# Performance work log

Hardware: AMD Instinct MI355X
Metric: run time of the kernel (lower is better)

Reference implementation:

```python
import jax, jax.numpy as jnp
import numpy as np

B, S, HID = 16, 577, 768
H, D = 12, 64          # heads, head_dim
N_KEEP = 576           # kept channels after structured pruning


def setup_inputs() -> dict:
    key = jax.random.key(0)
    ks = jax.random.split(key, 10)
    hs = jax.random.normal(ks[0], (B, S, HID), dtype=jnp.float32)
    Wq = jax.random.normal(ks[1], (HID, N_KEEP), dtype=jnp.float32) * 0.02
    bq = jax.random.normal(ks[2], (N_KEEP,), dtype=jnp.float32) * 0.02
    Wk = jax.random.normal(ks[3], (HID, N_KEEP), dtype=jnp.float32) * 0.02
    bk = jax.random.normal(ks[4], (N_KEEP,), dtype=jnp.float32) * 0.02
    Wv = jax.random.normal(ks[5], (HID, N_KEEP), dtype=jnp.float32) * 0.02
    bv = jax.random.normal(ks[6], (N_KEEP,), dtype=jnp.float32) * 0.02
    # positions of nonzero entries of the boolean padding masks (unique, sorted)
    q_idx = jnp.sort(jax.random.permutation(ks[7], HID)[:N_KEEP]).astype(jnp.int32)
    k_idx = jnp.sort(jax.random.permutation(ks[8], HID)[:N_KEEP]).astype(jnp.int32)
    v_idx = jnp.sort(jax.random.permutation(ks[9], HID)[:N_KEEP]).astype(jnp.int32)
    return {"hidden_states": hs, "Wq": Wq, "bq": bq, "Wk": Wk, "bk": bk,
            "Wv": Wv, "bv": bv, "q_idx": q_idx, "k_idx": k_idx, "v_idx": v_idx}


def _pad_and_split_heads(x, idx):
    # scatter pruned channels [B,S,N_KEEP] back into full layout [B,S,HID],
    # then split into heads -> [B,H,S,D]
    padded = jnp.zeros((B, S, HID), dtype=x.dtype).at[:, :, idx].set(x)
    return padded.reshape(B, S, H, D).transpose(0, 2, 1, 3)


def reference(hidden_states, Wq, bq, Wk, bk, Wv, bv, q_idx, k_idx, v_idx):
    q = hidden_states @ Wq + bq            # [B,S,N_KEEP]
    k = hidden_states @ Wk + bk
    v = hidden_states @ Wv + bv
    ql = _pad_and_split_heads(q, q_idx)     # [B,H,S,D]
    kl = _pad_and_split_heads(k, k_idx)
    vl = _pad_and_split_heads(v, v_idx)
    scale = 1.0 / np.float32(np.sqrt(D))
    scores = jnp.einsum('bhqd,bhkd->bhqk', ql, kl) * scale  # [B,H,S,S]
    probs = jax.nn.softmax(scores, axis=-1)
    ctx = jnp.einsum('bhqk,bhkd->bhqd', probs, vl)          # [B,H,S,D]
    ctx = ctx.transpose(0, 2, 1, 3).reshape(B, S, HID)       # [B,S,HID]
    return ctx[:, :, v_idx]                                  # gather kept channels
```

## Files before the change

### kernel.cpp

```cpp
#include <hip/hip_runtime.h>
#include <hip/hip_bf16.h>
#include <cstdint>
#include <cstddef>

#define B_     16
#define S_     577
#define HID_   768
#define H_     12
#define D_     64
#define NKEEP_ 576
#define MROWS  (B_ * S_)
#define BHROWS (B_ * H_ * S_)

typedef __bf16 bf16;
typedef __bf16 bf16x8 __attribute__((ext_vector_type(8)));
typedef float  f32x4  __attribute__((ext_vector_type(4)));

__device__ __forceinline__ void gload16(const bf16* g, bf16* l) {
    __builtin_amdgcn_global_load_lds(
        (const __attribute__((address_space(1))) unsigned int*)g,
        (__attribute__((address_space(3))) unsigned int*)l, 16, 0, 0);
}

__global__ __launch_bounds__(256) void k_cvt(const float* __restrict__ src,
                                             bf16* __restrict__ dst, int n4) {
    int i = blockIdx.x * 256 + threadIdx.x;
    if (i >= n4) return;
    float4 v = reinterpret_cast<const float4*>(src)[i];
    union { bf16 h[4]; uint2 u; } o;
    o.h[0] = (bf16)v.x; o.h[1] = (bf16)v.y; o.h[2] = (bf16)v.z; o.h[3] = (bf16)v.w;
    reinterpret_cast<uint2*>(dst)[i] = o.u;
}

__global__ void k_inv(const int* __restrict__ qi, const int* __restrict__ ki,
                      const int* __restrict__ vi,
                      const float* __restrict__ bq, const float* __restrict__ bk,
                      const float* __restrict__ bv,
                      int* __restrict__ inv, float* __restrict__ bias_p) {
    int p = blockIdx.x, t = threadIdx.x;
    inv[p * HID_ + t] = -1;
    bias_p[p * HID_ + t] = 0.0f;
    __syncthreads();
    const int* src = (p == 0) ? qi : (p == 1) ? ki : vi;
    const float* bb = (p == 0) ? bq : (p == 1) ? bk : bv;
    if (t < NKEEP_) {
        inv[p * HID_ + src[t]] = t;
        bias_p[p * HID_ + src[t]] = bb[t];
    }
}

__global__ __launch_bounds__(256) void k_wt(const float* __restrict__ Wq,
                                            const float* __restrict__ Wk,
                                            const float* __restrict__ Wv,
                                            const int* __restrict__ qi,
                                            const int* __restrict__ ki,
                                            const int* __restrict__ vi,
                                            bf16* __restrict__ Wp_t) {
    __shared__ float tile[64][33];
    const int p = blockIdx.y;
    const int j0 = blockIdx.x * 32;
    const float* W  = (p == 0) ? Wq : (p == 1) ? Wk : Wv;
    const int* idx  = (p == 0) ? qi : (p == 1) ? ki : vi;
    bf16* dst = Wp_t + (size_t)p * HID_ * HID_;
    const int t = threadIdx.x;
    const int lj = t & 31, lk = t >> 5;
    const int sj = t >> 3, ke = (t & 7) * 8;
    const int c = idx[j0 + sj];
    for (int kt = 0; kt < HID_; kt += 64) {
        __syncthreads();
#pragma unroll
        for (int i = 0; i < 8; ++i)
            tile[lk + i * 8][lj] = W[(size_t)(kt + lk + i * 8) * NKEEP_ + j0 + lj];
        __syncthreads();
        union { bf16 h[8]; bf16x8 v; } o;
#pragma unroll
        for (int i = 0; i < 8; ++i) o.h[i] = (bf16)tile[ke + i][sj];
        *reinterpret_cast<bf16x8*>(dst + (size_t)c * HID_ + kt + ke) = o.v;
    }
}

#define BM 128
#define BN 128
#define BK 32

__global__ __launch_bounds__(256) void k_gemm(const bf16* __restrict__ X,
                                              const bf16* __restrict__ Wp_t,
                                              const float* __restrict__ bias_p,
                                              bf16* __restrict__ Qo, bf16* __restrict__ Ko,
                                              bf16* __restrict__ Vo) {
    __shared__ bf16 smem[8448];
    bf16* Asm = smem;
    bf16* Bsm = smem + 4096;

    const int L = (blockIdx.x & 7) * 180 + (blockIdx.x >> 3);
    const int m_ = L / 18, np = L % 18;
    if (m_ >= 73) return;
    const int m0 = m_ * BM;
    const int n0 = (np % 6) * BN;
    const int p  = np / 6;

    const bf16* Wbase = Wp_t + (size_t)p * HID_ * HID_;
    bf16* Obase = (p == 0) ? Qo : (p == 1) ? Ko : Vo;
    const float osc = (p == 0) ? 0.125f : 1.0f;

    const int t = threadIdx.x;
    const int wid = t >> 6, lane = t & 63;
    const int wr = wid >> 1, wc = wid & 1;
    const int lrow = lane & 15, g = lane >> 4, lk = (lane >> 4) * 8;
    const int srow = lane >> 2, scol = (lane & 3) * 8;

    f32x4 acc[4][4] = {};

    for (int kk = 0; kk < HID_; kk += BK) {
        __syncthreads();
#pragma unroll
        for (int i = 0; i < 2; ++i) {
            const int c = wid * 2 + i;
            gload16(X + (size_t)(m0 + c * 16 + srow) * HID_ + kk + scol, Asm + c * 512);
            gload16(Wbase + (size_t)(n0 + c * 16 + srow) * HID_ + kk + scol, Bsm + c * 512);
        }
        __syncthreads();

        bf16x8 af[4], bfr[4];
#pragma unroll
        for (int m = 0; m < 4; ++m)
            af[m] = *reinterpret_cast<const bf16x8*>(&Asm[(wr * 64 + m * 16 + lrow) * BK + lk]);
#pragma unroll
        for (int n = 0; n < 4; ++n)
            bfr[n] = *reinterpret_cast<const bf16x8*>(&Bsm[(wc * 64 + n * 16 + lrow) * BK + lk]);
#pragma unroll
        for (int m = 0; m < 4; ++m)
#pragma unroll
            for (int n = 0; n < 4; ++n)
                acc[m][n] = __builtin_amdgcn_mfma_f32_16x16x32_bf16(af[m], bfr[n], acc[m][n], 0, 0, 0);
    }

    float bias_n[4];
#pragma unroll
    for (int n = 0; n < 4; ++n)
        bias_n[n] = bias_p[p * HID_ + n0 + wc * 64 + n * 16 + lrow];

    const int rowl = t >> 2, cq = t & 3;
#pragma unroll
    for (int half = 0; half < 2; ++half) {
        __syncthreads();
        if (wr == half) {
#pragma unroll
            for (int n = 0; n < 4; ++n)
#pragma unroll
                for (int m = 0; m < 4; ++m)
#pragma unroll
                    for (int r = 0; r < 4; ++r)
                        smem[(m * 16 + g * 4 + r) * 132 + wc * 64 + n * 16 + lrow] =
                            (bf16)((acc[m][n][r] + bias_n[n]) * osc);
        }
        __syncthreads();
        const int grow = m0 + half * 64 + rowl;
        if (grow < MROWS) {
            const int b = grow / S_, s = grow % S_;
            const size_t rbase = ((size_t)b * H_ * S_ + s) * D_;
#pragma unroll
            for (int i = 0; i < 4; ++i) {
                const int c0 = i * 32 + cq * 8;
                bf16x8 v = *reinterpret_cast<const bf16x8*>(&smem[rowl * 132 + c0]);
                const int c = n0 + c0, h = c >> 6, d = c & 63;
                *reinterpret_cast<bf16x8*>(&Obase[rbase + (size_t)h * S_ * D_ + d]) = v;
            }
        }
    }
}

#define KB2  64
#define VLD2 72

__global__ __launch_bounds__(512, 4) void k_attn(const bf16* __restrict__ Q,
                                                 const bf16* __restrict__ K,
                                                 const bf16* __restrict__ V,
                                                 const int* __restrict__ inv,
                                                 float* __restrict__ out) {
    __shared__ bf16 Ksm[KB2 * VLD2];
    __shared__ bf16 Vsm[D_ * VLD2];

    const int bid = blockIdx.x;
    const int bh = bid % (B_ * H_);
    const int q0 = (bid / (B_ * H_)) * 128;
    const int t = threadIdx.x, wid = t >> 6, lane = t & 63;
    const int lcol = lane & 15, g = lane >> 4;

    const bf16* Qb = Q + (size_t)bh * S_ * D_;
    const bf16* Kb = K + (size_t)bh * S_ * D_;
    const bf16* Vb = V + (size_t)bh * S_ * D_;

    const int qrow = q0 + wid * 16 + lcol;
    bf16x8 qf0 = {}, qf1 = {};
    if (qrow < S_) {
        qf0 = *reinterpret_cast<const bf16x8*>(Qb + (size_t)qrow * D_ + g * 8);
        qf1 = *reinterpret_cast<const bf16x8*>(Qb + (size_t)qrow * D_ + 32 + g * 8);
    }

    const int key_t = t >> 3;
    const int a_t = t & 7;
    const int ch_t = a_t * 8;
    const int ks_s = key_t >> 4, g_s = (key_t >> 2) & 3, r_s = key_t & 3;
    const int pos = (ks_s >> 1) * 32 + g_s * 8 + (ks_s & 1) * 4 + r_s;

    float mrun = -INFINITY, lrun = 0.f;
    f32x4 oT[4] = {};
    const bf16x8 zv = {};

    bf16x8 kreg = zv, vreg = zv;
    if (key_t < S_) {
        kreg = *reinterpret_cast<const bf16x8*>(Kb + (size_t)key_t * D_ + ch_t);
        vreg = *reinterpret_cast<const bf16x8*>(Vb + (size_t)key_t * D_ + ch_t);
    }

    for (int k0 = 0; k0 < S_; k0 += KB2) {
        __syncthreads();
        *reinterpret_cast<bf16x8*>(&Ksm[key_t * VLD2 + ch_t]) = kreg;
#pragma unroll
        for (int i = 0; i < 8; ++i) {
            int ch = (pos >> 3) ^ i ^ a_t;
            Vsm[(ch_t + i) * VLD2 + ch * 8 + (pos & 7)] = vreg[i];
        }
        __syncthreads();

        if (k0 + KB2 < S_) {
            int gk = k0 + KB2 + key_t;
            if (gk < S_) {
                kreg = *reinterpret_cast<const bf16x8*>(Kb + (size_t)gk * D_ + ch_t);
                vreg = *reinterpret_cast<const bf16x8*>(Vb + (size_t)gk * D_ + ch_t);
            } else { kreg = zv; vreg = zv; }
        }

        f32x4 sv[4];
#pragma unroll
        for (int ks = 0; ks < 4; ++ks) {
            const bf16* kr = &Ksm[(ks * 16 + lcol) * VLD2];
            bf16x8 kf0 = *reinterpret_cast<const bf16x8*>(kr + g * 8);
            bf16x8 kf1 = *reinterpret_cast<const bf16x8*>(kr + 32 + g * 8);
            f32x4 z = {};
            z = __builtin_amdgcn_mfma_f32_16x16x32_bf16(kf0, qf0, z, 0, 0, 0);
            z = __builtin_amdgcn_mfma_f32_16x16x32_bf16(kf1, qf1, z, 0, 0, 0);
            sv[ks] = z;
        }
        if (k0 + KB2 > S_) {
#pragma unroll
            for (int ks = 0; ks < 4; ++ks)
#pragma unroll
                for (int r = 0; r < 4; ++r)
                    if (k0 + ks * 16 + g * 4 + r >= S_) sv[ks][r] = -INFINITY;
        }

        float tm = sv[0][0];
#pragma unroll
        for (int ks = 0; ks < 4; ++ks)
#pragma unroll
            for (int r = 0; r < 4; ++r) tm = fmaxf(tm, sv[ks][r]);
        tm = fmaxf(tm, __shfl_xor(tm, 16));
        tm = fmaxf(tm, __shfl_xor(tm, 32));

        if (__any(tm > mrun + 8.f)) {
            float mnew = fmaxf(mrun, tm);
            float corr = __expf(mrun - mnew);
            mrun = mnew;
            lrun *= corr;
#pragma unroll
            for (int tt = 0; tt < 4; ++tt)
#pragma unroll
                for (int r = 0; r < 4; ++r) oT[tt][r] *= corr;
        }

        union { bf16 h[16]; bf16x8 v[2]; } pu;
        float rs = 0.f;
#pragma unroll
        for (int ks = 0; ks < 4; ++ks)
#pragma unroll
            for (int r = 0; r < 4; ++r) {
                float pv = __expf(sv[ks][r] - mrun);
                rs += pv;
                pu.h[ks * 4 + r] = (bf16)pv;
            }
        rs += __shfl_xor(rs, 16);
        rs += __shfl_xor(rs, 32);
        lrun += rs;

#pragma unroll
        for (int kh = 0; kh < 2; ++kh) {
#pragma unroll
            for (int tt = 0; tt < 4; ++tt) {
                int d = tt * 16 + lcol;
                int s3 = (d ^ (d >> 3)) & 7;
                int ch = (kh * 4 + g) ^ s3;
                bf16x8 vf = *reinterpret_cast<const bf16x8*>(&Vsm[d * VLD2 + ch * 8]);
                oT[tt] = __builtin_amdgcn_mfma_f32_16x16x32_bf16(vf, pu.v[kh], oT[tt], 0, 0, 0);
            }
        }
    }

    if (qrow < S_) {
        const int b = bh / H_, h = bh % H_;
        const int* invv = inv + 2 * HID_;
        float invl = 1.0f / lrun;
        float* orow = out + ((size_t)b * S_ + qrow) * NKEEP_;
#pragma unroll
        for (int tt = 0; tt < 4; ++tt)
#pragma unroll
            for (int r = 0; r < 4; ++r) {
                int d = tt * 16 + g * 4 + r;
                int j = invv[h * D_ + d];
                if (j >= 0) orow[j] = oT[tt][r] * invl;
            }
    }
}

extern "C" void kernel_launch(void* const* d_in, const int* in_sizes, int n_in,
                              void* d_out, int out_size, void* d_ws, size_t ws_size,
                              hipStream_t stream) {
    const float* hs = (const float*)d_in[0];
    const float* Wq = (const float*)d_in[1];
    const float* bq = (const float*)d_in[2];
    const float* Wk = (const float*)d_in[3];
    const float* bk = (const float*)d_in[4];
    const float* Wv = (const float*)d_in[5];
    const float* bv = (const float*)d_in[6];
    const int* qi = (const int*)d_in[7];
    const int* ki = (const int*)d_in[8];
    const int* vi = (const int*)d_in[9];
    float* out = (float*)d_out;

    char* ws = (char*)d_ws;
    size_t off = 0;
    bf16* hs_bf = (bf16*)(ws + off); off += (size_t)MROWS * HID_ * 2;
    bf16* Wp_t  = (bf16*)(ws + off); off += (size_t)3 * HID_ * HID_ * 2;
    float* bias_p = (float*)(ws + off); off += 3 * HID_ * 4;
    int* inv = (int*)(ws + off); off += 3 * HID_ * 4;
    bf16* Qw = (bf16*)(ws + off); off += (size_t)BHROWS * D_ * 2;
    bf16* Kw = (bf16*)(ws + off); off += (size_t)BHROWS * D_ * 2;
    bf16* Vw = (bf16*)(ws + off); off += (size_t)BHROWS * D_ * 2;

    const int n4 = MROWS * HID_ / 4;
    hipMemsetAsync(Wp_t, 0, (size_t)3 * HID_ * HID_ * 2, stream);
    k_cvt<<<(n4 + 255) / 256, 256, 0, stream>>>(hs, hs_bf, n4);
    k_inv<<<3, HID_, 0, stream>>>(qi, ki, vi, bq, bk, bv, inv, bias_p);
    k_wt<<<dim3(NKEEP_ / 32, 3), 256, 0, stream>>>(Wq, Wk, Wv, qi, ki, vi, Wp_t);
    k_gemm<<<1440, 256, 0, stream>>>(hs_bf, Wp_t, bias_p, Qw, Kw, Vw);
    k_attn<<<5 * B_ * H_, 512, 0, stream>>>(Qw, Kw, Vw, inv, out);
}
```

Baseline: 130.8 us.

## Triple-buffer GEMM LDS loads and double-buffer attention K/V tiles

The projection GEMM now uses a three-stage LDS ring with async global-to-LDS loads issued two tiles ahead. Each step waits with a manual vmcnt/barrier instead of two __syncthreads. The attention kernel double-buffers its K/V shared tiles, which removes one barrier per key block, and raises wave priority around the MFMA sections. This trades more LDS per block (48KB in the GEMM, double in attention), which may lower occupancy, for overlap of memory latency with compute.

```diff
diff --git a/kernel.cpp b/kernel.cpp
--- a/kernel.cpp
+++ b/kernel.cpp
@@ -21,6 +21,8 @@
         (const __attribute__((address_space(1))) unsigned int*)g,
         (__attribute__((address_space(3))) unsigned int*)l, 16, 0, 0);
 }
+
+#define WAITBAR(N) asm volatile("s_waitcnt vmcnt(" #N ") lgkmcnt(0)\n\ts_barrier" ::: "memory")
 
 __global__ __launch_bounds__(256) void k_cvt(const float* __restrict__ src,
                                              bf16* __restrict__ dst, int n4) {
@@ -82,15 +84,14 @@
 #define BM 128
 #define BN 128
 #define BK 32
+#define NT 24
 
 __global__ __launch_bounds__(256) void k_gemm(const bf16* __restrict__ X,
                                               const bf16* __restrict__ Wp_t,
                                               const float* __restrict__ bias_p,
                                               bf16* __restrict__ Qo, bf16* __restrict__ Ko,
                                               bf16* __restrict__ Vo) {
-    __shared__ bf16 smem[8448];
-    bf16* Asm = smem;
-    bf16* Bsm = smem + 4096;
+    __shared__ bf16 smem[24576];
 
     const int L = (blockIdx.x & 7) * 180 + (blockIdx.x >> 3);
     const int m_ = L / 18, np = L % 18;
@@ -109,31 +110,66 @@
     const int lrow = lane & 15, g = lane >> 4, lk = (lane >> 4) * 8;
     const int srow = lane >> 2, scol = (lane & 3) * 8;
 
+    const bf16* Xs = X + (size_t)m0 * HID_;
+    const bf16* Ws = Wbase + (size_t)n0 * HID_;
+
     f32x4 acc[4][4] = {};
 
-    for (int kk = 0; kk < HID_; kk += BK) {
-        __syncthreads();
-#pragma unroll
-        for (int i = 0; i < 2; ++i) {
-            const int c = wid * 2 + i;
-            gload16(X + (size_t)(m0 + c * 16 + srow) * HID_ + kk + scol, Asm + c * 512);
-            gload16(Wbase + (size_t)(n0 + c * 16 + srow) * HID_ + kk + scol, Bsm + c * 512);
-        }
-        __syncthreads();
-
-        bf16x8 af[4], bfr[4];
-#pragma unroll
-        for (int m = 0; m < 4; ++m)
-            af[m] = *reinterpret_cast<const bf16x8*>(&Asm[(wr * 64 + m * 16 + lrow) * BK + lk]);
-#pragma unroll
-        for (int n = 0; n < 4; ++n)
-            bfr[n] = *reinterpret_cast<const bf16x8*>(&Bsm[(wc * 64 + n * 16 + lrow) * BK + lk]);
-#pragma unroll
-        for (int m = 0; m < 4; ++m)
-#pragma unroll
-            for (int n = 0; n < 4; ++n)
-                acc[m][n] = __builtin_amdgcn_mfma_f32_16x16x32_bf16(af[m], bfr[n], acc[m][n], 0, 0, 0);
-    }
+#define STAGE(buf, kk)                                                          \
+    {                                                                           \
+        _Pragma("unroll")                                                       \
+        for (int i_ = 0; i_ < 2; ++i_) {                                        \
+            const int c_ = wid * 2 + i_;                                        \
+            gload16(Xs + (size_t)(c_ * 16 + srow) * HID_ + (kk) + scol,         \
+                    smem + (buf) * 8192 + c_ * 512);                            \
+            gload16(Ws + (size_t)(c_ * 16 + srow) * HID_ + (kk) + scol,         \
+                    smem + (buf) * 8192 + 4096 + c_ * 512);                     \
+        }                                                                       \
+    }
+
+#define COMPUTE(buf)                                                            \
+    {                                                                           \
+        const bf16* As_ = smem + (buf) * 8192;                                  \
+        const bf16* Bs_ = As_ + 4096;                                           \
+        bf16x8 af[4], bfr[4];                                                   \
+        _Pragma("unroll")                                                       \
+        for (int m = 0; m < 4; ++m)                                             \
+            af[m] = *reinterpret_cast<const bf16x8*>(                           \
+                &As_[(wr * 64 + m * 16 + lrow) * BK + lk]);                     \
+        _Pragma("unroll")                                                       \
+        for (int n = 0; n < 4; ++n)                                             \
+            bfr[n] = *reinterpret_cast<const bf16x8*>(                          \
+                &Bs_[(wc * 64 + n * 16 + lrow) * BK + lk]);                     \
+        _Pragma("unroll")                                                       \
+        for (int m = 0; m < 4; ++m)                                             \
+            _Pragma("unroll")                                                   \
+            for (int n = 0; n < 4; ++n)                                         \
+                acc[m][n] = __builtin_amdgcn_mfma_f32_16x16x32_bf16(            \
+                    af[m], bfr[n], acc[m][n], 0, 0, 0);                         \
+    }
+
+    STAGE(0, 0)
+    STAGE(1, BK)
+    WAITBAR(4);
+
+    int kk_next = 2 * BK;
+    for (int u = 0; u < 7; ++u) {
+#pragma unroll
+        for (int j = 0; j < 3; ++j) {
+            STAGE((j + 2) % 3, kk_next)
+            COMPUTE(j)
+            WAITBAR(4);
+            kk_next += BK;
+        }
+    }
+    STAGE(2, 23 * BK)
+    COMPUTE(0)
+    WAITBAR(4);
+    COMPUTE(1)
+    WAITBAR(0);
+    COMPUTE(2)
+#undef STAGE
+#undef COMPUTE
 
     float bias_n[4];
 #pragma unroll
@@ -172,14 +208,15 @@
 
 #define KB2  64
 #define VLD2 72
+#define KVSZ (KB2 * VLD2)
 
 __global__ __launch_bounds__(512, 4) void k_attn(const bf16* __restrict__ Q,
                                                  const bf16* __restrict__ K,
                                                  const bf16* __restrict__ V,
                                                  const int* __restrict__ inv,
                                                  float* __restrict__ out) {
-    __shared__ bf16 Ksm[KB2 * VLD2];
-    __shared__ bf16 Vsm[D_ * VLD2];
+    __shared__ bf16 Ksm[2][KVSZ];
+    __shared__ bf16 Vsm[2][KVSZ];
 
     const int bid = blockIdx.x;
     const int bh = bid % (B_ * H_);
@@ -214,13 +251,13 @@
         vreg = *reinterpret_cast<const bf16x8*>(Vb + (size_t)key_t * D_ + ch_t);
     }
 
+    int cur = 0;
     for (int k0 = 0; k0 < S_; k0 += KB2) {
-        __syncthreads();
-        *reinterpret_cast<bf16x8*>(&Ksm[key_t * VLD2 + ch_t]) = kreg;
+        *reinterpret_cast<bf16x8*>(&Ksm[cur][key_t * VLD2 + ch_t]) = kreg;
 #pragma unroll
         for (int i = 0; i < 8; ++i) {
             int ch = (pos >> 3) ^ i ^ a_t;
-            Vsm[(ch_t + i) * VLD2 + ch * 8 + (pos & 7)] = vreg[i];
+            Vsm[cur][(ch_t + i) * VLD2 + ch * 8 + (pos & 7)] = vreg[i];
         }
         __syncthreads();
 
@@ -233,9 +270,10 @@
         }
 
         f32x4 sv[4];
+        __builtin_amdgcn_s_setprio(1);
 #pragma unroll
         for (int ks = 0; ks < 4; ++ks) {
-            const bf16* kr = &Ksm[(ks * 16 + lcol) * VLD2];
+            const bf16* kr = &Ksm[cur][(ks * 16 + lcol) * VLD2];
             bf16x8 kf0 = *reinterpret_cast<const bf16x8*>(kr + g * 8);
             bf16x8 kf1 = *reinterpret_cast<const bf16x8*>(kr + 32 + g * 8);
             f32x4 z = {};
@@ -243,6 +281,7 @@
             z = __builtin_amdgcn_mfma_f32_16x16x32_bf16(kf1, qf1, z, 0, 0, 0);
             sv[ks] = z;
         }
+        __builtin_amdgcn_s_setprio(0);
         if (k0 + KB2 > S_) {
 #pragma unroll
             for (int ks = 0; ks < 4; ++ks)
@@ -284,6 +323,7 @@
         rs += __shfl_xor(rs, 32);
         lrun += rs;
 
+        __builtin_amdgcn_s_setprio(1);
 #pragma unroll
         for (int kh = 0; kh < 2; ++kh) {
 #pragma unroll
@@ -291,10 +331,12 @@
                 int d = tt * 16 + lcol;
                 int s3 = (d ^ (d >> 3)) & 7;
                 int ch = (kh * 4 + g) ^ s3;
-                bf16x8 vf = *reinterpret_cast<const bf16x8*>(&Vsm[d * VLD2 + ch * 8]);
+                bf16x8 vf = *reinterpret_cast<const bf16x8*>(&Vsm[cur][d * VLD2 + ch * 8]);
                 oT[tt] = __builtin_amdgcn_mfma_f32_16x16x32_bf16(vf, pu.v[kh], oT[tt], 0, 0, 0);
             }
         }
+        __builtin_amdgcn_s_setprio(0);
+        cur ^= 1;
     }
 
     if (qrow < S_) {
```

Result: faster. 126.0 us (-3.7%).
